# Optimization experiments

Hardware: AMD Instinct MI355X
Metric: run time of the kernel (lower is better)

The kernel has to match this reference:

```python
import jax, jax.numpy as jnp
import numpy as np

B, C, N, K, L = 4, 256, 8192, 4, 3


def _mlp2(h, W1, b1, W2, b2):
    return jax.nn.relu(h @ W1 + b1) @ W2 + b2


def setup_inputs() -> dict:
    key = jax.random.key(0)
    ks = jax.random.split(key, 12)
    s = lambda fan_in: 1.0 / np.sqrt(fan_in)
    inp = {
        "x": jax.random.normal(ks[0], (B, C, N), jnp.float32),
        "points": jax.random.normal(ks[1], (N, 3), jnp.float32),
        "neighbors": jax.random.randint(ks[2], (N, K), 0, N, jnp.int32),
        "edge_W1": jax.random.normal(ks[3], (3, C // 4), jnp.float32) * s(3),
        "edge_b1": jnp.zeros((C // 4,), jnp.float32),
        "edge_W2": jax.random.normal(ks[4], (C // 4, C // 2), jnp.float32) * s(C // 4),
        "edge_b2": jnp.zeros((C // 2,), jnp.float32),
        "msg_W1": jax.random.normal(ks[5], (L, 2 * C + C // 2, 2 * C), jnp.float32) * s(2 * C + C // 2),
        "msg_b1": jnp.zeros((L, 2 * C), jnp.float32),
        "msg_W2": jax.random.normal(ks[6], (L, 2 * C, C), jnp.float32) * s(2 * C),
        "msg_b2": jnp.zeros((L, C), jnp.float32),
        "upd_W1": jax.random.normal(ks[7], (L, 2 * C, 2 * C), jnp.float32) * s(2 * C),
        "upd_b1": jnp.zeros((L, 2 * C), jnp.float32),
        "upd_W2": jax.random.normal(ks[8], (L, 2 * C, C), jnp.float32) * s(2 * C),
        "upd_b2": jnp.zeros((L, C), jnp.float32),
    }
    return inp


def reference(x, points, neighbors, edge_W1, edge_b1, edge_W2, edge_b2,
              msg_W1, msg_b1, msg_W2, msg_b2, upd_W1, upd_b1, upd_W2, upd_b2):
    # x: [B, C, N] -> features [B, N, C]
    feats = jnp.transpose(x, (0, 2, 1))
    # edge features shared across layers: [N, K, C//2]
    edge_vec = points[neighbors] - points[:, None, :]          # [N, K, 3]
    edge_feat = _mlp2(edge_vec, edge_W1, edge_b1, edge_W2, edge_b2)
    for l in range(L):
        sender = feats[:, neighbors, :]                         # [B, N, K, C]
        receiver = jnp.broadcast_to(feats[:, :, None, :], sender.shape)
        ef = jnp.broadcast_to(edge_feat[None], (feats.shape[0],) + edge_feat.shape)
        msg_in = jnp.concatenate([sender, receiver, ef], axis=-1)  # [B,N,K,2.5C]
        msg = _mlp2(msg_in, msg_W1[l], msg_b1[l], msg_W2[l], msg_b2[l])
        agg = jnp.mean(msg, axis=2)                             # [B, N, C]
        upd_in = jnp.concatenate([feats, agg], axis=-1)         # [B, N, 2C]
        feats = _mlp2(upd_in, upd_W1[l], upd_b1[l], upd_W2[l], upd_b2[l])
    return jnp.transpose(feats, (0, 2, 1))
```

## Files before the change

### kernel.cpp

```cpp
#include <hip/hip_runtime.h>

#define DEVI __device__ __forceinline__

typedef unsigned short u16;
typedef unsigned int   u32;
typedef __attribute__((ext_vector_type(8))) short short8;
typedef __attribute__((ext_vector_type(4))) short short4b;
typedef __attribute__((ext_vector_type(4))) float f32x4;

DEVI float bf2f(u16 u) {
    union { u32 i; float f; } x; x.i = ((u32)u) << 16; return x.f;
}
DEVI u16 f2bf(float f) {
    u32 u = __float_as_uint(f);
    u32 r = (u + 0x7FFFu + ((u >> 16) & 1u)) >> 16;
    return (u16)r;
}

DEVI void gload_lds16(const void* g, void* l) {
    __builtin_amdgcn_global_load_lds((const __attribute__((address_space(1))) void*)g,
                                     (__attribute__((address_space(3))) void*)l, 16, 0, 0);
}

struct PJob { u32 dst, soff, tbase, ld, Kd, src; };
__device__ const PJob g_jobs[19] = {
    {0,        0,      0,    128, 64,  4},
    {8192,     0,      8,    512, 256, 0},
    {139264,   131072, 136,  512, 256, 0},
    {270336,   262144, 264,  512, 128, 0},
    {335872,   0,      328,  256, 512, 1},
    {466944,   0,      456,  512, 512, 2},
    {729088,   0,      712,  256, 512, 3},
    {860160,   327680, 840,  512, 256, 0},
    {991232,   458752, 968,  512, 256, 0},
    {1122304,  589824, 1096, 512, 128, 0},
    {1187840,  131072, 1160, 256, 512, 1},
    {1318912,  262144, 1288, 512, 512, 2},
    {1581056,  131072, 1544, 256, 512, 3},
    {1712128,  655360, 1672, 512, 256, 0},
    {1843200,  786432, 1800, 512, 256, 0},
    {1974272,  917504, 1928, 512, 128, 0},
    {2039808,  262144, 1992, 256, 512, 1},
    {2170880,  524288, 2120, 512, 512, 2},
    {2433024,  262144, 2376, 256, 512, 3},
};

__global__ void prep_weights(const float* __restrict__ mW1, const float* __restrict__ mW2,
                             const float* __restrict__ uW1, const float* __restrict__ uW2,
                             const float* __restrict__ eW2, u16* __restrict__ wreg)
{
    int bid = blockIdx.x;
    int ji = 0;
    #pragma unroll
    for (int i = 1; i < 19; ++i) if (bid >= (int)g_jobs[i].tbase) ji = i;
    PJob jb = g_jobs[ji];
    const float* src = (jb.src == 0) ? mW1 : (jb.src == 1) ? mW2 : (jb.src == 2) ? uW1
                     : (jb.src == 3) ? uW2 : eW2;
    src += jb.soff;
    int t  = bid - (int)jb.tbase;
    int nk = (int)jb.Kd >> 5;
    int tk = t % nk, tj = t / nk;
    int k0 = tk * 32, j0 = tj * 32;
    __shared__ float tile[32][33];
    int tx = threadIdx.x, ty = threadIdx.y;
    #pragma unroll
    for (int yy = 0; yy < 4; ++yy) {
        int k = k0 + ty + yy * 8;
        tile[ty + yy * 8][tx] = src[(size_t)k * jb.ld + j0 + tx];
    }
    __syncthreads();
    u16* dst = wreg + jb.dst;
    #pragma unroll
    for (int yy = 0; yy < 4; ++yy) {
        int j = j0 + ty + yy * 8;
        dst[(size_t)j * jb.Kd + k0 + tx] = f2bf(tile[tx][ty + yy * 8]);
    }
}

__global__ __launch_bounds__(256) void conv_w2(const float* __restrict__ mW2,
                                               u16* __restrict__ mW2bf)
{
    int i = blockIdx.x * 256 + threadIdx.x;
    float4 v = *(const float4*)&mW2[(size_t)i * 4];
    short4b o;
    o[0] = (short)f2bf(v.x); o[1] = (short)f2bf(v.y);
    o[2] = (short)f2bf(v.z); o[3] = (short)f2bf(v.w);
    *(short4b*)&mW2bf[(size_t)i * 4] = o;
}

__global__ __launch_bounds__(256) void biasfix(const u16* __restrict__ wreg,
    const float* __restrict__ mb2, const float* __restrict__ ub1,
    float* __restrict__ ub1c)
{
    int idx = blockIdx.x * 256 + threadIdx.x;
    int l = idx >> 9, n = idx & 511;
    const u16* U1T = wreg + 8192 + l * 851968 + 458752;
    const float* b2 = mb2 + l * 256;
    float s = ub1[l * 512 + n];
    for (int j0 = 0; j0 < 256; j0 += 8) {
        short8 wv = *(const short8*)&U1T[(size_t)n * 512 + 256 + j0];
        #pragma unroll
        for (int jj = 0; jj < 8; ++jj) s += bf2f((u16)wv[jj]) * b2[j0 + jj];
    }
    ub1c[idx] = s;
}

__global__ void transpose_in(const float* __restrict__ x, u16* __restrict__ feats)
{
    __shared__ float tile[32][33];
    int n0 = blockIdx.x * 32, c0 = blockIdx.y * 32, b = blockIdx.z;
    int tx = threadIdx.x, ty = threadIdx.y;
    #pragma unroll
    for (int yy = 0; yy < 4; ++yy) {
        int c = c0 + ty + yy * 8;
        tile[ty + yy * 8][tx] = x[((size_t)b * 256 + c) * 8192 + n0 + tx];
    }
    __syncthreads();
    #pragma unroll
    for (int yy = 0; yy < 4; ++yy) {
        int n = n0 + ty + yy * 8;
        feats[((size_t)b * 8192 + n) * 256 + c0 + tx] = f2bf(tile[tx][ty + yy * 8]);
    }
}

__global__ void transpose_out(const u16* __restrict__ feats, float* __restrict__ out)
{
    __shared__ float tile[32][33];
    int n0 = blockIdx.x * 32, c0 = blockIdx.y * 32, b = blockIdx.z;
    int tx = threadIdx.x, ty = threadIdx.y;
    #pragma unroll
    for (int yy = 0; yy < 4; ++yy) {
        int n = n0 + ty + yy * 8;
        tile[ty + yy * 8][tx] = bf2f(feats[((size_t)b * 8192 + n) * 256 + c0 + tx]);
    }
    __syncthreads();
    #pragma unroll
    for (int yy = 0; yy < 4; ++yy) {
        int c = c0 + ty + yy * 8;
        out[((size_t)b * 256 + c) * 8192 + n0 + tx] = tile[tx][ty + yy * 8];
    }
}

__global__ __launch_bounds__(256) void edge_h(
    const float* __restrict__ points, const int* __restrict__ nb,
    const float* __restrict__ W1, const float* __restrict__ b1,
    u16* __restrict__ h)
{
    int e = blockIdx.x * 256 + threadIdx.x;
    int n = e >> 2;
    int j2 = nb[e];
    float p0x = points[n * 3], p0y = points[n * 3 + 1], p0z = points[n * 3 + 2];
    float v0 = points[j2 * 3]     - p0x;
    float v1 = points[j2 * 3 + 1] - p0y;
    float v2 = points[j2 * 3 + 2] - p0z;
    #pragma unroll
    for (int jb = 0; jb < 8; ++jb) {
        short8 o;
        #pragma unroll
        for (int jj = 0; jj < 8; ++jj) {
            int j = jb * 8 + jj;
            float hv = v0 * W1[j] + v1 * W1[64 + j] + v2 * W1[128 + j] + b1[j];
            o[jj] = (short)f2bf(fmaxf(hv, 0.0f));
        }
        *(short8*)&h[(size_t)e * 64 + jb * 8] = o;
    }
}

__global__ __launch_bounds__(512, 4) void gemm_bt(
    const u16* __restrict__ A1, int lda1, int K1,
    const u16* __restrict__ A2, int lda2,
    const u16* __restrict__ B1, int ldb1,
    const u16* __restrict__ B2, int ldb2,
    const float* __restrict__ bias,
    u16* __restrict__ Cp, int ldc,
    int nbn, int Ktot, int relu, int permrows,
    long sA, long sB, long sC)
{
    __shared__ u16 lds[32768];
    {
        long by = blockIdx.y;
        A1 += by * sA; A2 += by * sA;
        B1 += by * sB; B2 += by * sB;
        Cp += by * sC;
    }
    int nwg = (int)gridDim.x;
    int bx0 = (int)blockIdx.x;
    int bx = (bx0 & 7) * (nwg >> 3) + (bx0 >> 3);
    int tn = bx % nbn, tm = bx / nbn;
    int t = threadIdx.x;
    int l = t & 63, w = t >> 6;
    int wrow = (w >> 2) * 64, wcol = (w & 3) * 32;
    int lm = l & 15, lk = l >> 4;
    int swz = lm & 7;
    int rowA = tm * 128;
    int rowB = tn * 128;

    f32x4 acc[4][2];
    #pragma unroll
    for (int mi = 0; mi < 4; ++mi)
        #pragma unroll
        for (int ni = 0; ni < 2; ++ni)
            acc[mi][ni] = (f32x4){0.f, 0.f, 0.f, 0.f};

    auto STAGE = [&](int d, int ks) {
        int kg0 = ks << 6;
        bool useA1 = kg0 < K1;
        const u16* Ab = useA1 ? A1 : A2;
        const u16* Bb = useA1 ? B1 : B2;
        int lda = useA1 ? lda1 : lda2;
        int ldb = useA1 ? ldb1 : ldb2;
        int kg  = useA1 ? kg0 : kg0 - K1;
        u16* At = lds + d * 16384;
        u16* Bt = At + 8192;
        #pragma unroll
        for (int i = 0; i < 2; ++i) {
            int chunk = i * 512 + t;
            int r = chunk >> 3, s = chunk & 7;
            int c = s ^ (r & 7);
            gload_lds16(Ab + (size_t)(rowA + r) * lda + kg + c * 8, &At[chunk * 8]);
        }
        #pragma unroll
        for (int i = 0; i < 2; ++i) {
            int chunk = i * 512 + t;
            int r = chunk >> 3, s = chunk & 7;
            int c = s ^ (r & 7);
            gload_lds16(Bb + (size_t)(rowB + r) * ldb + kg + c * 8, &Bt[chunk * 8]);
        }
    };

    int nks = Ktot >> 6;
    STAGE(0, 0);
    if (nks > 1) STAGE(1, 1);
    int cur = 0;
    for (int ks = 0; ks < nks; ++ks) {
        if (ks + 1 < nks) asm volatile("s_waitcnt vmcnt(4)\n\ts_barrier" ::: "memory");
        else              asm volatile("s_waitcnt vmcnt(0)\n\ts_barrier" ::: "memory");
        const u16* At = lds + cur * 16384;
        const u16* Bt = At + 8192;
        __builtin_amdgcn_s_setprio(1);
        #pragma unroll
        for (int ksub = 0; ksub < 2; ++ksub) {
            int sOff = (((ksub << 2) | lk) ^ swz) << 3;
            short8 af[4], bv[2];
            #pragma unroll
            for (int mi = 0; mi < 4; ++mi)
                af[mi] = *(const short8*)&At[(wrow + mi * 16 + lm) * 64 + sOff];
            #pragma unroll
            for (int ni = 0; ni < 2; ++ni)
                bv[ni] = *(const short8*)&Bt[(wcol + ni * 16 + lm) * 64 + sOff];
            #pragma unroll
            for (int mi = 0; mi < 4; ++mi)
                #pragma unroll
                for (int ni = 0; ni < 2; ++ni)
                    acc[mi][ni] = __builtin_amdgcn_mfma_f32_16x16x32_bf16(af[mi], bv[ni], acc[mi][ni], 0, 0, 0);
        }
        __builtin_amdgcn_s_setprio(0);
        asm volatile("s_barrier" ::: "memory");
        if (ks + 2 < nks) STAGE(cur, ks + 2);
        cur ^= 1;
    }

    #pragma unroll
    for (int ni = 0; ni < 2; ++ni) {
        int col = wcol + ni * 16 + lm;
        float bvl = bias ? bias[tn * 128 + col] : 0.0f;
        #pragma unroll
        for (int mi = 0; mi < 4; ++mi) {
            int row0 = wrow + mi * 16 + lk * 4;
            f32x4 v = acc[mi][ni];
            #pragma unroll
            for (int r = 0; r < 4; ++r) {
                float f = v[r] + bvl;
                if (relu) f = fmaxf(f, 0.0f);
                lds[(row0 + r) * 136 + col] = f2bf(f);
            }
        }
    }
    __syncthreads();
    #pragma unroll
    for (int p = 0; p < 4; ++p) {
        int chunk = p * 512 + t;
        int row = chunk >> 4, sl = chunk & 15;
        short8 v = *(const short8*)&lds[row * 136 + sl * 8];
        int m = tm * 128 + row;
        int orow = permrows ? (((m & 8191) << 2) | (m >> 13)) : m;
        *(short8*)&Cp[(size_t)orow * ldc + tn * 128 + sl * 8] = v;
    }
}

__global__ __launch_bounds__(256) void gather_relu_mean(
    const u16* __restrict__ PR, const u16* __restrict__ E,
    const int* __restrict__ nb, const float* __restrict__ b1,
    u16* __restrict__ hbar)
{
    int b = threadIdx.x >> 6, l = threadIdx.x & 63;
    int c0 = l * 8;
    int n0 = blockIdx.x * 4;

    float4 b1a = *(const float4*)&b1[c0];
    float4 b1b = *(const float4*)&b1[c0 + 4];
    float bb[8] = {b1a.x, b1a.y, b1a.z, b1a.w, b1b.x, b1b.y, b1b.z, b1b.w};

    int4 nbv[4];
    #pragma unroll
    for (int ii = 0; ii < 4; ++ii) nbv[ii] = *(const int4*)&nb[(n0 + ii) * 4];

    #pragma unroll
    for (int ii = 0; ii < 4; ++ii) {
        int n = n0 + ii;
        int nbarr[4] = {nbv[ii].x, nbv[ii].y, nbv[ii].z, nbv[ii].w};

        short8 rv = *(const short8*)&PR[(size_t)(n * 4 + b) * 1024 + 512 + c0];
        float base[8], acc[8];
        #pragma unroll
        for (int j = 0; j < 8; ++j) { base[j] = bf2f((u16)rv[j]) + bb[j]; acc[j] = 0.0f; }

        #pragma unroll
        for (int k = 0; k < 4; ++k) {
            short8 pv = *(const short8*)&PR[(size_t)(nbarr[k] * 4 + b) * 1024 + c0];
            short8 ev = *(const short8*)&E[(size_t)(n * 4 + k) * 512 + c0];
            #pragma unroll
            for (int j = 0; j < 8; ++j) {
                float v = bf2f((u16)pv[j]) + bf2f((u16)ev[j]) + base[j];
                acc[j] += fmaxf(v, 0.0f);
            }
        }
        short8 o;
        #pragma unroll
        for (int j = 0; j < 8; ++j) o[j] = (short)f2bf(acc[j] * 0.25f);
        *(short8*)&hbar[((size_t)(b << 13) + n) * 512 + c0] = o;
    }
}

extern "C" void kernel_launch(void* const* d_in, const int* in_sizes, int n_in,
                              void* d_out, int out_size, void* d_ws, size_t ws_size,
                              hipStream_t stream)
{
    const float* x      = (const float*)d_in[0];
    const float* points = (const float*)d_in[1];
    const int*   nb     = (const int*)d_in[2];
    const float* eW1    = (const float*)d_in[3];
    const float* eb1    = (const float*)d_in[4];
    const float* eW2    = (const float*)d_in[5];
    const float* eb2    = (const float*)d_in[6];
    const float* mW1    = (const float*)d_in[7];
    const float* mb1    = (const float*)d_in[8];
    const float* mW2    = (const float*)d_in[9];
    const float* mb2    = (const float*)d_in[10];
    const float* uW1    = (const float*)d_in[11];
    const float* ub1    = (const float*)d_in[12];
    const float* uW2    = (const float*)d_in[13];
    const float* ub2    = (const float*)d_in[14];
    float* out = (float*)d_out;

    char* ws = (char*)d_ws;
    u16* featsA = (u16*)(ws);
    u16* featsB = (u16*)(ws + 16777216);
    u16* ef     = (u16*)(ws + 33554432);
    u16* PR     = (u16*)(ws + 41943040);
    u16* E      = (u16*)(ws + 109051904);
    u16* hbar   = (u16*)(ws + 142606336);
    u16* wreg   = (u16*)(ws + 176160768);
    u16*   mW2bf = (u16*)(ws + 181288960);
    u16*   WcT   = (u16*)(ws + 182075392);
    float* ub1c  = (float*)(ws + 183648256);
    u16* hEdge  = PR;
    u16* H2     = PR;
    u16* agg    = E;

    const bool fused = (ws_size >= 183654400ull);

    prep_weights<<<2504, dim3(32, 8), 0, stream>>>(mW1, mW2, uW1, uW2, eW2, wreg);
    transpose_in<<<dim3(256, 8, 4), dim3(32, 8), 0, stream>>>(x, featsA);
    edge_h<<<128, 256, 0, stream>>>(points, nb, eW1, eb1, hEdge);
    gemm_bt<<<256, 512, 0, stream>>>(hEdge, 64, 64, hEdge, 64,
                                     wreg, 64, wreg, 64, eb2, ef, 128, 1, 64, 0, 0,
                                     0, 0, 0);

    if (fused) {
        conv_w2<<<384, 256, 0, stream>>>(mW2, mW2bf);
        {
            const u16* U1T0 = wreg + 8192 + 458752;
            gemm_bt<<<dim3(16, 3), 512, 0, stream>>>(U1T0 + 256, 512, 256, U1T0, 512,
                                                     mW2bf, 256, mW2bf, 256,
                                                     nullptr, WcT, 512, 4, 256, 0, 0,
                                                     851968, 131072, 262144);
        }
        biasfix<<<6, 256, 0, stream>>>(wreg, mb2, ub1, ub1c);
    }

    const u16* fin = featsA; u16* fout = featsB;
    for (int lyr = 0; lyr < 3; ++lyr) {
        u16* W1abT = wreg + 8192 + lyr * 851968;
        u16* W1cT  = W1abT + 262144;
        u16* W2T   = W1abT + 327680;
        u16* U1T   = W1abT + 458752;
        u16* U2T   = W1abT + 720896;
        const float* b1  = mb1 + lyr * 512;
        const float* b2  = mb2 + lyr * 256;
        const float* u1b = ub1 + lyr * 512;
        const float* u2b = ub2 + lyr * 256;

        gemm_bt<<<2048, 512, 0, stream>>>((const u16*)fin, 256, 256, (const u16*)fin, 256,
                                          W1abT, 256, W1abT, 256,
                                          nullptr, PR, 1024, 8, 256, 0, 1, 0, 0, 0);
        gemm_bt<<<1024, 512, 0, stream>>>(ef, 128, 128, ef, 128,
                                          W1cT, 128, W1cT, 128,
                                          nullptr, E, 512, 4, 128, 0, 0, 0, 0, 0);
        gather_relu_mean<<<2048, 256, 0, stream>>>(PR, E, nb, b1, hbar);

        if (fused) {
            gemm_bt<<<1024, 512, 0, stream>>>((const u16*)fin, 256, 256, hbar, 512,
                                              U1T, 512, WcT + lyr * 262144, 512,
                                              ub1c + lyr * 512, H2, 512, 4, 768, 1, 0,
                                              0, 0, 0);
        } else {
            gemm_bt<<<512, 512, 0, stream>>>(hbar, 512, 512, hbar, 512,
                                             W2T, 512, W2T, 512,
                                             b2, agg, 256, 2, 512, 0, 0, 0, 0, 0);
            gemm_bt<<<1024, 512, 0, stream>>>((const u16*)fin, 256, 256, agg, 256,
                                              U1T, 512, U1T + 256, 512,
                                              u1b, H2, 512, 4, 512, 1, 0, 0, 0, 0);
        }
        gemm_bt<<<512, 512, 0, stream>>>(H2, 512, 512, H2, 512,
                                         U2T, 512, U2T, 512,
                                         u2b, fout, 256, 2, 512, 0, 0, 0, 0, 0);

        const u16* tmp = fin; fin = fout; fout = (u16*)tmp;
    }
    transpose_out<<<dim3(256, 8, 4), dim3(32, 8), 0, stream>>>(fin, out);
}
```

Baseline: 434.3 us.

## Merge setup kernels, batch PR/E GEMMs into one launch, hoist gather loads

The separate weight-prep, input-transpose, edge-MLP hidden and W2-conversion kernels are combined into one setup kernel that branches on block index. The PR and E GEMMs of each layer now run as a single grouped launch with two argument sets. The GEMM staging now uses incrementally advanced pointers instead of recomputing addresses each stage. gather_relu_mean issues all neighbour and receiver loads up front to expose more memory parallelism and gets an occupancy hint. The aim is fewer launches and more loads in flight, at the cost of higher register pressure in the gather and branch divergence in the combined setup kernel.

```diff
diff --git a/kernel.cpp b/kernel.cpp
--- a/kernel.cpp
+++ b/kernel.cpp
@@ -45,47 +45,86 @@
     {2433024,  262144, 2376, 256, 512, 3},
 };
 
-__global__ void prep_weights(const float* __restrict__ mW1, const float* __restrict__ mW2,
-                             const float* __restrict__ uW1, const float* __restrict__ uW2,
-                             const float* __restrict__ eW2, u16* __restrict__ wreg)
-{
+__global__ __launch_bounds__(256) void setup_kernel(
+    const float* __restrict__ x, u16* __restrict__ feats,
+    const float* __restrict__ points, const int* __restrict__ nb,
+    const float* __restrict__ eW1, const float* __restrict__ eb1,
+    u16* __restrict__ hEdge,
+    const float* __restrict__ mW1, const float* __restrict__ mW2,
+    const float* __restrict__ uW1, const float* __restrict__ uW2,
+    const float* __restrict__ eW2,
+    u16* __restrict__ wreg, u16* __restrict__ mW2bf)
+{
+    __shared__ float tile[32][33];
     int bid = blockIdx.x;
-    int ji = 0;
-    #pragma unroll
-    for (int i = 1; i < 19; ++i) if (bid >= (int)g_jobs[i].tbase) ji = i;
-    PJob jb = g_jobs[ji];
-    const float* src = (jb.src == 0) ? mW1 : (jb.src == 1) ? mW2 : (jb.src == 2) ? uW1
-                     : (jb.src == 3) ? uW2 : eW2;
-    src += jb.soff;
-    int t  = bid - (int)jb.tbase;
-    int nk = (int)jb.Kd >> 5;
-    int tk = t % nk, tj = t / nk;
-    int k0 = tk * 32, j0 = tj * 32;
-    __shared__ float tile[32][33];
-    int tx = threadIdx.x, ty = threadIdx.y;
-    #pragma unroll
-    for (int yy = 0; yy < 4; ++yy) {
-        int k = k0 + ty + yy * 8;
-        tile[ty + yy * 8][tx] = src[(size_t)k * jb.ld + j0 + tx];
-    }
-    __syncthreads();
-    u16* dst = wreg + jb.dst;
-    #pragma unroll
-    for (int yy = 0; yy < 4; ++yy) {
-        int j = j0 + ty + yy * 8;
-        dst[(size_t)j * jb.Kd + k0 + tx] = f2bf(tile[tx][ty + yy * 8]);
-    }
-}
-
-__global__ __launch_bounds__(256) void conv_w2(const float* __restrict__ mW2,
-                                               u16* __restrict__ mW2bf)
-{
-    int i = blockIdx.x * 256 + threadIdx.x;
-    float4 v = *(const float4*)&mW2[(size_t)i * 4];
-    short4b o;
-    o[0] = (short)f2bf(v.x); o[1] = (short)f2bf(v.y);
-    o[2] = (short)f2bf(v.z); o[3] = (short)f2bf(v.w);
-    *(short4b*)&mW2bf[(size_t)i * 4] = o;
+    int t = threadIdx.x;
+    int tx = t & 31, ty = t >> 5;
+
+    if (bid < 2504) {
+        int ji = 0;
+        #pragma unroll
+        for (int i = 1; i < 19; ++i) if (bid >= (int)g_jobs[i].tbase) ji = i;
+        PJob jb = g_jobs[ji];
+        const float* src = (jb.src == 0) ? mW1 : (jb.src == 1) ? mW2 : (jb.src == 2) ? uW1
+                         : (jb.src == 3) ? uW2 : eW2;
+        src += jb.soff;
+        int tt = bid - (int)jb.tbase;
+        int nk = (int)jb.Kd >> 5;
+        int tk = tt % nk, tj = tt / nk;
+        int k0 = tk * 32, j0 = tj * 32;
+        #pragma unroll
+        for (int yy = 0; yy < 4; ++yy) {
+            int k = k0 + ty + yy * 8;
+            tile[ty + yy * 8][tx] = src[(size_t)k * jb.ld + j0 + tx];
+        }
+        __syncthreads();
+        u16* dst = wreg + jb.dst;
+        #pragma unroll
+        for (int yy = 0; yy < 4; ++yy) {
+            int j = j0 + ty + yy * 8;
+            dst[(size_t)j * jb.Kd + k0 + tx] = f2bf(tile[tx][ty + yy * 8]);
+        }
+    } else if (bid < 10696) {
+        int bb = bid - 2504;
+        int n0 = (bb & 255) * 32, c0 = ((bb >> 8) & 7) * 32, b = bb >> 11;
+        #pragma unroll
+        for (int yy = 0; yy < 4; ++yy) {
+            int c = c0 + ty + yy * 8;
+            tile[ty + yy * 8][tx] = x[((size_t)b * 256 + c) * 8192 + n0 + tx];
+        }
+        __syncthreads();
+        #pragma unroll
+        for (int yy = 0; yy < 4; ++yy) {
+            int n = n0 + ty + yy * 8;
+            feats[((size_t)b * 8192 + n) * 256 + c0 + tx] = f2bf(tile[tx][ty + yy * 8]);
+        }
+    } else if (bid < 10824) {
+        int e = (bid - 10696) * 256 + t;
+        int n = e >> 2;
+        int j2 = nb[e];
+        float p0x = points[n * 3], p0y = points[n * 3 + 1], p0z = points[n * 3 + 2];
+        float v0 = points[j2 * 3]     - p0x;
+        float v1 = points[j2 * 3 + 1] - p0y;
+        float v2 = points[j2 * 3 + 2] - p0z;
+        #pragma unroll
+        for (int jb2 = 0; jb2 < 8; ++jb2) {
+            short8 o;
+            #pragma unroll
+            for (int jj = 0; jj < 8; ++jj) {
+                int j = jb2 * 8 + jj;
+                float hv = v0 * eW1[j] + v1 * eW1[64 + j] + v2 * eW1[128 + j] + eb1[j];
+                o[jj] = (short)f2bf(fmaxf(hv, 0.0f));
+            }
+            *(short8*)&hEdge[(size_t)e * 64 + jb2 * 8] = o;
+        }
+    } else {
+        int i = (bid - 10824) * 256 + t;
+        float4 v = *(const float4*)&mW2[(size_t)i * 4];
+        short4b o;
+        o[0] = (short)f2bf(v.x); o[1] = (short)f2bf(v.y);
+        o[2] = (short)f2bf(v.z); o[3] = (short)f2bf(v.w);
+        *(short4b*)&mW2bf[(size_t)i * 4] = o;
+    }
 }
 
 __global__ __launch_bounds__(256) void biasfix(const u16* __restrict__ wreg,
@@ -105,31 +144,13 @@
     ub1c[idx] = s;
 }
 
-__global__ void transpose_in(const float* __restrict__ x, u16* __restrict__ feats)
+__global__ void transpose_out(const u16* __restrict__ feats, float* __restrict__ out)
 {
     __shared__ float tile[32][33];
     int n0 = blockIdx.x * 32, c0 = blockIdx.y * 32, b = blockIdx.z;
     int tx = threadIdx.x, ty = threadIdx.y;
     #pragma unroll
     for (int yy = 0; yy < 4; ++yy) {
-        int c = c0 + ty + yy * 8;
-        tile[ty + yy * 8][tx] = x[((size_t)b * 256 + c) * 8192 + n0 + tx];
-    }
-    __syncthreads();
-    #pragma unroll
-    for (int yy = 0; yy < 4; ++yy) {
-        int n = n0 + ty + yy * 8;
-        feats[((size_t)b * 8192 + n) * 256 + c0 + tx] = f2bf(tile[tx][ty + yy * 8]);
-    }
-}
-
-__global__ void transpose_out(const u16* __restrict__ feats, float* __restrict__ out)
-{
-    __shared__ float tile[32][33];
-    int n0 = blockIdx.x * 32, c0 = blockIdx.y * 32, b = blockIdx.z;
-    int tx = threadIdx.x, ty = threadIdx.y;
-    #pragma unroll
-    for (int yy = 0; yy < 4; ++yy) {
         int n = n0 + ty + yy * 8;
         tile[ty + yy * 8][tx] = bf2f(feats[((size_t)b * 8192 + n) * 256 + c0 + tx]);
     }
@@ -141,52 +162,33 @@
     }
 }
 
-__global__ __launch_bounds__(256) void edge_h(
-    const float* __restrict__ points, const int* __restrict__ nb,
-    const float* __restrict__ W1, const float* __restrict__ b1,
-    u16* __restrict__ h)
-{
-    int e = blockIdx.x * 256 + threadIdx.x;
-    int n = e >> 2;
-    int j2 = nb[e];
-    float p0x = points[n * 3], p0y = points[n * 3 + 1], p0z = points[n * 3 + 2];
-    float v0 = points[j2 * 3]     - p0x;
-    float v1 = points[j2 * 3 + 1] - p0y;
-    float v2 = points[j2 * 3 + 2] - p0z;
-    #pragma unroll
-    for (int jb = 0; jb < 8; ++jb) {
-        short8 o;
-        #pragma unroll
-        for (int jj = 0; jj < 8; ++jj) {
-            int j = jb * 8 + jj;
-            float hv = v0 * W1[j] + v1 * W1[64 + j] + v2 * W1[128 + j] + b1[j];
-            o[jj] = (short)f2bf(fmaxf(hv, 0.0f));
-        }
-        *(short8*)&h[(size_t)e * 64 + jb * 8] = o;
-    }
-}
+struct GArgs {
+    const u16* A1; const u16* A2; const u16* B1; const u16* B2;
+    const float* bias; u16* C;
+    int lda1, K1, lda2, ldb1, ldb2, ldc, nbn, Ktot, relu, permrows;
+};
 
 __global__ __launch_bounds__(512, 4) void gemm_bt(
-    const u16* __restrict__ A1, int lda1, int K1,
-    const u16* __restrict__ A2, int lda2,
-    const u16* __restrict__ B1, int ldb1,
-    const u16* __restrict__ B2, int ldb2,
-    const float* __restrict__ bias,
-    u16* __restrict__ Cp, int ldc,
-    int nbn, int Ktot, int relu, int permrows,
-    long sA, long sB, long sC)
+    GArgs g0, GArgs g1, int nbx0, long sA, long sB, long sC)
 {
     __shared__ u16 lds[32768];
+    int bx0 = (int)blockIdx.x;
+    bool j0 = bx0 < nbx0;
+    GArgs g = j0 ? g0 : g1;
+    int nwgj = j0 ? nbx0 : ((int)gridDim.x - nbx0);
+    int bxl  = j0 ? bx0 : bx0 - nbx0;
+    int bx = (bxl & 7) * (nwgj >> 3) + (bxl >> 3);
+
+    const u16* A1 = g.A1; const u16* A2 = g.A2;
+    const u16* B1 = g.B1; const u16* B2 = g.B2;
+    u16* Cp = g.C;
     {
         long by = blockIdx.y;
         A1 += by * sA; A2 += by * sA;
         B1 += by * sB; B2 += by * sB;
         Cp += by * sC;
     }
-    int nwg = (int)gridDim.x;
-    int bx0 = (int)blockIdx.x;
-    int bx = (bx0 & 7) * (nwg >> 3) + (bx0 >> 3);
-    int tn = bx % nbn, tm = bx / nbn;
+    int tn = bx % g.nbn, tm = bx / g.nbn;
     int t = threadIdx.x;
     int l = t & 63, w = t >> 6;
     int wrow = (w >> 2) * 64, wcol = (w & 3) * 32;
@@ -202,35 +204,41 @@
         for (int ni = 0; ni < 2; ++ni)
             acc[mi][ni] = (f32x4){0.f, 0.f, 0.f, 0.f};
 
-    auto STAGE = [&](int d, int ks) {
-        int kg0 = ks << 6;
-        bool useA1 = kg0 < K1;
-        const u16* Ab = useA1 ? A1 : A2;
-        const u16* Bb = useA1 ? B1 : B2;
-        int lda = useA1 ? lda1 : lda2;
-        int ldb = useA1 ? ldb1 : ldb2;
-        int kg  = useA1 ? kg0 : kg0 - K1;
-        u16* At = lds + d * 16384;
+    int nks  = g.Ktot >> 6;
+    int nksw = (g.K1 < g.Ktot) ? (g.K1 >> 6) : 0x7fffffff;
+
+    int rr[2], cc[2];
+    const u16* pA[2]; const u16* pB[2];
+    #pragma unroll
+    for (int i = 0; i < 2; ++i) {
+        int chunk = i * 512 + t;
+        rr[i] = chunk >> 3;
+        cc[i] = (chunk & 7) ^ (rr[i] & 7);
+        pA[i] = A1 + (size_t)(rowA + rr[i]) * g.lda1 + cc[i] * 8;
+        pB[i] = B1 + (size_t)(rowB + rr[i]) * g.ldb1 + cc[i] * 8;
+    }
+    int st = 0;
+    auto STAGE = [&]() {
+        if (st == nksw) {
+            #pragma unroll
+            for (int i = 0; i < 2; ++i) {
+                pA[i] = A2 + (size_t)(rowA + rr[i]) * g.lda2 + cc[i] * 8;
+                pB[i] = B2 + (size_t)(rowB + rr[i]) * g.ldb2 + cc[i] * 8;
+            }
+        }
+        u16* At = lds + (st & 1) * 16384;
         u16* Bt = At + 8192;
         #pragma unroll
         for (int i = 0; i < 2; ++i) {
             int chunk = i * 512 + t;
-            int r = chunk >> 3, s = chunk & 7;
-            int c = s ^ (r & 7);
-            gload_lds16(Ab + (size_t)(rowA + r) * lda + kg + c * 8, &At[chunk * 8]);
-        }
-        #pragma unroll
-        for (int i = 0; i < 2; ++i) {
-            int chunk = i * 512 + t;
-            int r = chunk >> 3, s = chunk & 7;
-            int c = s ^ (r & 7);
-            gload_lds16(Bb + (size_t)(rowB + r) * ldb + kg + c * 8, &Bt[chunk * 8]);
-        }
+            gload_lds16(pA[i], &At[chunk * 8]); pA[i] += 64;
+            gload_lds16(pB[i], &Bt[chunk * 8]); pB[i] += 64;
+        }
+        ++st;
     };
 
-    int nks = Ktot >> 6;
-    STAGE(0, 0);
-    if (nks > 1) STAGE(1, 1);
+    STAGE();
+    if (nks > 1) STAGE();
     int cur = 0;
     for (int ks = 0; ks < nks; ++ks) {
         if (ks + 1 < nks) asm volatile("s_waitcnt vmcnt(4)\n\ts_barrier" ::: "memory");
@@ -256,14 +264,14 @@
         }
         __builtin_amdgcn_s_setprio(0);
         asm volatile("s_barrier" ::: "memory");
-        if (ks + 2 < nks) STAGE(cur, ks + 2);
+        if (st < nks) STAGE();
         cur ^= 1;
     }
 
     #pragma unroll
     for (int ni = 0; ni < 2; ++ni) {
         int col = wcol + ni * 16 + lm;
-        float bvl = bias ? bias[tn * 128 + col] : 0.0f;
+        float bvl = g.bias ? g.bias[tn * 128 + col] : 0.0f;
         #pragma unroll
         for (int mi = 0; mi < 4; ++mi) {
             int row0 = wrow + mi * 16 + lk * 4;
@@ -271,7 +279,7 @@
             #pragma unroll
             for (int r = 0; r < 4; ++r) {
                 float f = v[r] + bvl;
-                if (relu) f = fmaxf(f, 0.0f);
+                if (g.relu) f = fmaxf(f, 0.0f);
                 lds[(row0 + r) * 136 + col] = f2bf(f);
             }
         }
@@ -283,12 +291,12 @@
         int row = chunk >> 4, sl = chunk & 15;
         short8 v = *(const short8*)&lds[row * 136 + sl * 8];
         int m = tm * 128 + row;
-        int orow = permrows ? (((m & 8191) << 2) | (m >> 13)) : m;
-        *(short8*)&Cp[(size_t)orow * ldc + tn * 128 + sl * 8] = v;
-    }
-}
-
-__global__ __launch_bounds__(256) void gather_relu_mean(
+        int orow = g.permrows ? (((m & 8191) << 2) | (m >> 13)) : m;
+        *(short8*)&Cp[(size_t)orow * g.ldc + tn * 128 + sl * 8] = v;
+    }
+}
+
+__global__ __launch_bounds__(256, 3) void gather_relu_mean(
     const u16* __restrict__ PR, const u16* __restrict__ E,
     const int* __restrict__ nb, const float* __restrict__ b1,
     u16* __restrict__ hbar)
@@ -297,31 +305,44 @@
     int c0 = l * 8;
     int n0 = blockIdx.x * 4;
 
+    int nbarr[4][4];
+    #pragma unroll
+    for (int ii = 0; ii < 4; ++ii) {
+        int4 v = *(const int4*)&nb[(n0 + ii) * 4];
+        nbarr[ii][0] = v.x; nbarr[ii][1] = v.y; nbarr[ii][2] = v.z; nbarr[ii][3] = v.w;
+    }
+
+    short8 pv[4][4];
+    #pragma unroll
+    for (int ii = 0; ii < 4; ++ii)
+        #pragma unroll
+        for (int k = 0; k < 4; ++k)
+            pv[ii][k] = *(const short8*)&PR[(size_t)(nbarr[ii][k] * 4 + b) * 1024 + c0];
+    short8 rv[4];
+    #pragma unroll
+    for (int ii = 0; ii < 4; ++ii)
+        rv[ii] = *(const short8*)&PR[(size_t)((n0 + ii) * 4 + b) * 1024 + 512 + c0];
+
     float4 b1a = *(const float4*)&b1[c0];
     float4 b1b = *(const float4*)&b1[c0 + 4];
     float bb[8] = {b1a.x, b1a.y, b1a.z, b1a.w, b1b.x, b1b.y, b1b.z, b1b.w};
 
-    int4 nbv[4];
-    #pragma unroll
-    for (int ii = 0; ii < 4; ++ii) nbv[ii] = *(const int4*)&nb[(n0 + ii) * 4];
-
     #pragma unroll
     for (int ii = 0; ii < 4; ++ii) {
         int n = n0 + ii;
-        int nbarr[4] = {nbv[ii].x, nbv[ii].y, nbv[ii].z, nbv[ii].w};
-
-        short8 rv = *(const short8*)&PR[(size_t)(n * 4 + b) * 1024 + 512 + c0];
+        short8 ev[4];
+        #pragma unroll
+        for (int k = 0; k < 4; ++k)
+            ev[k] = *(const short8*)&E[(size_t)(n * 4 + k) * 512 + c0];
+
         float base[8], acc[8];
         #pragma unroll
-        for (int j = 0; j < 8; ++j) { base[j] = bf2f((u16)rv[j]) + bb[j]; acc[j] = 0.0f; }
-
+        for (int j = 0; j < 8; ++j) { base[j] = bf2f((u16)rv[ii][j]) + bb[j]; acc[j] = 0.0f; }
         #pragma unroll
         for (int k = 0; k < 4; ++k) {
-            short8 pv = *(const short8*)&PR[(size_t)(nbarr[k] * 4 + b) * 1024 + c0];
-            short8 ev = *(const short8*)&E[(size_t)(n * 4 + k) * 512 + c0];
             #pragma unroll
             for (int j = 0; j < 8; ++j) {
-                float v = bf2f((u16)pv[j]) + bf2f((u16)ev[j]) + base[j];
+                float v = bf2f((u16)pv[ii][k][j]) + bf2f((u16)ev[k][j]) + base[j];
                 acc[j] += fmaxf(v, 0.0f);
             }
         }
@@ -330,6 +351,18 @@
         for (int j = 0; j < 8; ++j) o[j] = (short)f2bf(acc[j] * 0.25f);
         *(short8*)&hbar[((size_t)(b << 13) + n) * 512 + c0] = o;
     }
+}
+
+static inline GArgs mkargs(const u16* A1, int lda1, int K1, const u16* A2, int lda2,
+                           const u16* B1, int ldb1, const u16* B2, int ldb2,
+                           const float* bias, u16* C, int ldc,
+                           int nbn, int Ktot, int relu, int permrows)
+{
+    GArgs g;
+    g.A1 = A1; g.A2 = A2; g.B1 = B1; g.B2 = B2; g.bias = bias; g.C = C;
+    g.lda1 = lda1; g.K1 = K1; g.lda2 = lda2; g.ldb1 = ldb1; g.ldb2 = ldb2;
+    g.ldc = ldc; g.nbn = nbn; g.Ktot = Ktot; g.relu = relu; g.permrows = permrows;
+    return g;
 }
 
 extern "C" void kernel_launch(void* const* d_in, const int* in_sizes, int n_in,
@@ -370,22 +403,21 @@
 
     const bool fused = (ws_size >= 183654400ull);
 
-    prep_weights<<<2504, dim3(32, 8), 0, stream>>>(mW1, mW2, uW1, uW2, eW2, wreg);
-    transpose_in<<<dim3(256, 8, 4), dim3(32, 8), 0, stream>>>(x, featsA);
-    edge_h<<<128, 256, 0, stream>>>(points, nb, eW1, eb1, hEdge);
-    gemm_bt<<<256, 512, 0, stream>>>(hEdge, 64, 64, hEdge, 64,
-                                     wreg, 64, wreg, 64, eb2, ef, 128, 1, 64, 0, 0,
-                                     0, 0, 0);
+    setup_kernel<<<fused ? 11208 : 10824, 256, 0, stream>>>(
+        x, featsA, points, nb, eW1, eb1, hEdge,
+        mW1, mW2, uW1, uW2, eW2, wreg, mW2bf);
+
+    {
+        GArgs g = mkargs(hEdge, 64, 64, hEdge, 64, wreg, 64, wreg, 64,
+                         eb2, ef, 128, 1, 64, 0, 0);
+        gemm_bt<<<256, 512, 0, stream>>>(g, g, 256, 0, 0, 0);
+    }
 
     if (fused) {
-        conv_w2<<<384, 256, 0, stream>>>(mW2, mW2bf);
-        {
-            const u16* U1T0 = wreg + 8192 + 458752;
-            gemm_bt<<<dim3(16, 3), 512, 0, stream>>>(U1T0 + 256, 512, 256, U1T0, 512,
-                                                     mW2bf, 256, mW2bf, 256,
-                                                     nullptr, WcT, 512, 4, 256, 0, 0,
-                                                     851968, 131072, 262144);
-        }
+        const u16* U1T0 = wreg + 8192 + 458752;
+        GArgs g = mkargs(U1T0 + 256, 512, 256, U1T0, 512, mW2bf, 256, mW2bf, 256,
+                         nullptr, WcT, 512, 4, 256, 0, 0);
+        gemm_bt<<<dim3(16, 3), 512, 0, stream>>>(g, g, 16, 851968, 131072, 262144);
         biasfix<<<6, 256, 0, stream>>>(wreg, mb2, ub1, ub1c);
     }
 
@@ -401,30 +433,34 @@
         const float* u1b = ub1 + lyr * 512;
         const float* u2b = ub2 + lyr * 256;
 
-        gemm_bt<<<2048, 512, 0, stream>>>((const u16*)fin, 256, 256, (const u16*)fin, 256,
-                                          W1abT, 256, W1abT, 256,
-                                          nullptr, PR, 1024, 8, 256, 0, 1, 0, 0, 0);
-        gemm_bt<<<1024, 512, 0, stream>>>(ef, 128, 128, ef, 128,
-                                          W1cT, 128, W1cT, 128,
-                                          nullptr, E, 512, 4, 128, 0, 0, 0, 0, 0);
+        {
+            GArgs gPR = mkargs((const u16*)fin, 256, 256, (const u16*)fin, 256,
+                               W1abT, 256, W1abT, 256, nullptr, PR, 1024, 8, 256, 0, 1);
+            GArgs gE  = mkargs(ef, 128, 128, ef, 128, W1cT, 128, W1cT, 128,
+                               nullptr, E, 512, 4, 128, 0, 0);
+            gemm_bt<<<3072, 512, 0, stream>>>(gPR, gE, 2048, 0, 0, 0);
+        }
         gather_relu_mean<<<2048, 256, 0, stream>>>(PR, E, nb, b1, hbar);
 
         if (fused) {
-            gemm_bt<<<1024, 512, 0, stream>>>((const u16*)fin, 256, 256, hbar, 512,
-                                              U1T, 512, WcT + lyr * 262144, 512,
-                                              ub1c + lyr * 512, H2, 512, 4, 768, 1, 0,
-                                              0, 0, 0);
+            GArgs g = mkargs((const u16*)fin, 256, 256, hbar, 512,
+                             U1T, 512, WcT + lyr * 262144, 512,
+                             ub1c + lyr * 512, H2, 512, 4, 768, 1, 0);
+            gemm_bt<<<1024, 512, 0, stream>>>(g, g, 1024, 0, 0, 0);
         } else {
-            gemm_bt<<<512, 512, 0, stream>>>(hbar, 512, 512, hbar, 512,
-                                             W2T, 512, W2T, 512,
-                                             b2, agg, 256, 2, 512, 0, 0, 0, 0, 0);
-            gemm_bt<<<1024, 512, 0, stream>>>((const u16*)fin, 256, 256, agg, 256,
-                                              U1T, 512, U1T + 256, 512,
-                                              u1b, H2, 512, 4, 512, 1, 0, 0, 0, 0);
-        }
-        gemm_bt<<<512, 512, 0, stream>>>(H2, 512, 512, H2, 512,
-                                         U2T, 512, U2T, 512,
-                                         u2b, fout, 256, 2, 512, 0, 0, 0, 0, 0);
+            GArgs ga = mkargs(hbar, 512, 512, hbar, 512, W2T, 512, W2T, 512,
+                              b2, agg, 256, 2, 512, 0, 0);
+            gemm_bt<<<512, 512, 0, stream>>>(ga, ga, 512, 0, 0, 0);
+            GArgs gh = mkargs((const u16*)fin, 256, 256, agg, 256,
+                              U1T, 512, U1T + 256, 512,
+                              u1b, H2, 512, 4, 512, 1, 0);
+            gemm_bt<<<1024, 512, 0, stream>>>(gh, gh, 1024, 0, 0, 0);
+        }
+        {
+            GArgs g = mkargs(H2, 512, 512, H2, 512, U2T, 512, U2T, 512,
+                             u2b, fout, 256, 2, 512, 0, 0);
+            gemm_bt<<<512, 512, 0, stream>>>(g, g, 512, 0, 0, 0);
+        }
 
         const u16* tmp = fin; fin = fout; fout = (u16*)tmp;
     }
```

After: 409.2 us. 5.8% less time.
